# Kernel optimization log

Measured on AMD Instinct MI355X. Metric: run time of the kernel, lower is better.

Reference implementation:

```python
import jax, jax.numpy as jnp
import numpy as np

MOMENTUM = 0.5  # update_method='momentum'
EPS = 1e-12


def _l2norm(x):
    return x / jnp.sqrt(jnp.sum(x * x, axis=-1, keepdims=True) + EPS)


def setup_inputs() -> dict:
    key = jax.random.key(0)
    k1, k2, k3, k4, k5 = jax.random.split(key, 5)
    N, D, C, B = 200000, 256, 1000, 256
    inputs = _l2norm(jax.random.normal(k1, (B, D), dtype=jnp.float32))
    features = _l2norm(jax.random.normal(k2, (N, D), dtype=jnp.float32))
    cluster_mean = jax.random.normal(k3, (C, D), dtype=jnp.float32)
    labels = jax.random.randint(k4, (N,), 0, C)
    indexes = jax.random.randint(k5, (B,), 0, N)
    targets = labels[indexes]  # cluster id of each mini-batch sample
    return {
        "inputs": inputs,
        "features": features,
        "cluster_mean": cluster_mean,
        "indexes": indexes,
        "labels": labels,
        "targets": targets,
    }


def reference(inputs, features, cluster_mean, indexes, labels, targets):
    # HM.forward: logits against cluster centroids
    outputs = inputs @ cluster_mean.T  # [B, C]

    # HM.backward side effects (memory-bank maintenance), vectorized:
    # 1) momentum scatter update of the per-instance memory bank + L2 renorm
    new_rows = MOMENTUM * features[indexes] + (1.0 - MOMENTUM) * inputs
    new_rows = _l2norm(new_rows)
    feats = features.at[indexes].set(new_rows)

    # 2) naive cluster-mean recompute (get_mean_conv mean part) for touched clusters
    C = cluster_mean.shape[0]
    sums = jax.ops.segment_sum(feats, labels, num_segments=C)            # [C, D]
    cnts = jax.ops.segment_sum(jnp.ones((feats.shape[0],), feats.dtype), labels, num_segments=C)
    means = sums / jnp.maximum(cnts, 1.0)[:, None]
    touched = jnp.zeros((C,), dtype=bool).at[targets].set(True)
    new_cluster_mean = jnp.where(touched[:, None], means, cluster_mean)

    return outputs, feats, new_cluster_mean
```

## Files before the change

kernel.cpp:

```cpp
#include <hip/hip_runtime.h>

typedef float f32x4 __attribute__((ext_vector_type(4)));

#define B 256
#define D 256
#define N 200000
#define C 1000

#define K1_BLOCKS   2048
#define LOGITS_LO   0
#define NEWROWS_LO  256
#define TOUCH_BLK   512
#define HIST_LO     513
#define HIST_BLOCKS 64
#define COPY_LO     577
#define COPY_BLOCKS (K1_BLOCKS - COPY_LO)

#define WS_NEWROWS_OFF  0
#define WS_HIST_OFF     262144
#define WS_TOUCHED_OFF  266144
#define WS_OFFS_OFF     270144
#define WS_FILLPOS_OFF  274144
#define WS_ROWLIST_OFF  278144
#define ZERO_WORDS      (2 * C)

__global__ __launch_bounds__(256) void k0_zero(int* __restrict__ z) {
    int i = blockIdx.x * 256 + threadIdx.x;
    if (i < ZERO_WORDS) z[i] = 0;
}

__global__ __launch_bounds__(256) void k1_kernel(
    const float* __restrict__ inputs, const float* __restrict__ features,
    const float* __restrict__ cluster_mean, const int* __restrict__ indexes,
    const int* __restrict__ labels, const int* __restrict__ targets,
    float* __restrict__ out_logits, float* __restrict__ out_feats,
    float* __restrict__ new_rows, int* __restrict__ hist, int* __restrict__ touched)
{
    const int blk = blockIdx.x;
    const int t = threadIdx.x;

    if (blk >= COPY_LO) {
        const f32x4* src = (const f32x4*)features;
        f32x4*       dst = (f32x4*)out_feats;
        const int total4 = N * (D / 4);
        const int stride = COPY_BLOCKS * 256;
        int i = (blk - COPY_LO) * 256 + t;
        for (; i + 3 * stride < total4; i += 4 * stride) {
            f32x4 v0 = src[i];
            f32x4 v1 = src[i + stride];
            f32x4 v2 = src[i + 2 * stride];
            f32x4 v3 = src[i + 3 * stride];
            __builtin_nontemporal_store(v0, dst + i);
            __builtin_nontemporal_store(v1, dst + i + stride);
            __builtin_nontemporal_store(v2, dst + i + 2 * stride);
            __builtin_nontemporal_store(v3, dst + i + 3 * stride);
        }
        for (; i < total4; i += stride)
            __builtin_nontemporal_store(src[i], dst + i);
    } else if (blk < NEWROWS_LO) {
        __shared__ float sbuf[D];
        int b = blk - LOGITS_LO;
        sbuf[t] = inputs[b * D + t];
        __syncthreads();
        const f32x4* cmv = (const f32x4*)cluster_mean;
        for (int c = t; c < C; c += 256) {
            const f32x4* cm = cmv + (size_t)c * 64;
            float a0 = 0.f, a1 = 0.f, a2 = 0.f, a3 = 0.f;
            #pragma unroll 8
            for (int d4 = 0; d4 < 64; ++d4) {
                f32x4 v = cm[d4];
                const float* si = sbuf + d4 * 4;
                a0 += v.x * si[0];
                a1 += v.y * si[1];
                a2 += v.z * si[2];
                a3 += v.w * si[3];
            }
            out_logits[(size_t)b * C + c] = (a0 + a1) + (a2 + a3);
        }
    } else if (blk < TOUCH_BLK) {
        __shared__ float wpart[4];
        __shared__ float stot;
        int b = blk - NEWROWS_LO;
        int r = indexes[b];
        float x = 0.5f * features[(size_t)r * D + t] + 0.5f * inputs[b * D + t];
        float s = x * x;
        #pragma unroll
        for (int off = 32; off > 0; off >>= 1) s += __shfl_down(s, off);
        if ((t & 63) == 0) wpart[t >> 6] = s;
        __syncthreads();
        if (t == 0) stot = (wpart[0] + wpart[1]) + (wpart[2] + wpart[3]);
        __syncthreads();
        new_rows[b * D + t] = x / sqrtf(stot + 1e-12f);
    } else if (blk == TOUCH_BLK) {
        if (t < B) touched[targets[t]] = 1;
    } else {
        __shared__ int lh[C];
        for (int i = t; i < C; i += 256) lh[i] = 0;
        __syncthreads();
        const int stride = HIST_BLOCKS * 256;
        for (int i = (blk - HIST_LO) * 256 + t; i < N; i += stride)
            atomicAdd(&lh[labels[i]], 1);
        __syncthreads();
        for (int i = t; i < C; i += 256) {
            int v = lh[i];
            if (v) atomicAdd(&hist[i], v);
        }
    }
}

__global__ __launch_bounds__(256) void k2_kernel(
    const int* __restrict__ indexes, const float* __restrict__ new_rows,
    float* __restrict__ out_feats, const int* __restrict__ hist,
    int* __restrict__ offs, int* __restrict__ fillpos)
{
    const int blk = blockIdx.x;
    const int t = threadIdx.x;

    if (blk < 256) {
        __shared__ int sidx[B];
        __shared__ int lose;
        sidx[t] = indexes[t];
        if (t == 0) lose = 0;
        __syncthreads();
        int b = blk;
        int my = sidx[b];
        if (t > b && sidx[t] == my) lose = 1;
        __syncthreads();
        if (!lose) out_feats[(size_t)my * D + t] = new_rows[b * D + t];
    } else {
        __shared__ int swt[4];
        int base = t * 4;
        int h0 = (base + 0 < C) ? hist[base + 0] : 0;
        int h1 = (base + 1 < C) ? hist[base + 1] : 0;
        int h2 = (base + 2 < C) ? hist[base + 2] : 0;
        int h3 = (base + 3 < C) ? hist[base + 3] : 0;
        int tot = h0 + h1 + h2 + h3;
        int lane = t & 63;
        int scan = tot;
        #pragma unroll
        for (int off = 1; off < 64; off <<= 1) {
            int v = __shfl_up(scan, off);
            if (lane >= off) scan += v;
        }
        if (lane == 63) swt[t >> 6] = scan;
        __syncthreads();
        int wbase = 0;
        for (int i = 0; i < (t >> 6); ++i) wbase += swt[i];
        int excl = wbase + scan - tot;
        if (base + 0 < C) { offs[base + 0] = excl;                fillpos[base + 0] = excl; }
        if (base + 1 < C) { offs[base + 1] = excl + h0;           fillpos[base + 1] = excl + h0; }
        if (base + 2 < C) { offs[base + 2] = excl + h0 + h1;      fillpos[base + 2] = excl + h0 + h1; }
        if (base + 3 < C) { offs[base + 3] = excl + h0 + h1 + h2; fillpos[base + 3] = excl + h0 + h1 + h2; }
    }
}

__global__ __launch_bounds__(256) void fill_kernel(
    const int* __restrict__ labels, const int* __restrict__ touched,
    int* __restrict__ fillpos, int* __restrict__ rowlist)
{
    int i = blockIdx.x * 256 + threadIdx.x;
    if (i >= N) return;
    int lab = labels[i];
    if (touched[lab]) {
        int p = atomicAdd(&fillpos[lab], 1);
        rowlist[p] = i;
    }
}

__global__ __launch_bounds__(1024) void cm_kernel(
    const float* __restrict__ cluster_mean, const float* __restrict__ out_feats,
    const int* __restrict__ touched, const int* __restrict__ hist,
    const int* __restrict__ offs, const int* __restrict__ rowlist,
    float* __restrict__ out_cm)
{
    const int c = blockIdx.x;
    const int d = threadIdx.x & 255;
    const int k = threadIdx.x >> 8;
    if (!touched[c]) {
        if (k == 0) out_cm[(size_t)c * D + d] = cluster_mean[(size_t)c * D + d];
        return;
    }
    __shared__ float red[3][256];
    const int cnt = hist[c];
    const int off = offs[c];
    float acc = 0.0f;
    #pragma unroll 4
    for (int j = k; j < cnt; j += 4)
        acc += out_feats[(size_t)rowlist[off + j] * D + d];
    if (k > 0) red[k - 1][d] = acc;
    __syncthreads();
    if (k == 0) {
        float tot = acc + red[0][d] + red[1][d] + red[2][d];
        out_cm[(size_t)c * D + d] = tot / fmaxf((float)cnt, 1.0f);
    }
}

extern "C" void kernel_launch(void* const* d_in, const int* in_sizes, int n_in,
                              void* d_out, int out_size, void* d_ws, size_t ws_size,
                              hipStream_t stream) {
    const float* inputs       = (const float*)d_in[0];
    const float* features     = (const float*)d_in[1];
    const float* cluster_mean = (const float*)d_in[2];
    const int*   indexes      = (const int*)d_in[3];
    const int*   labels       = (const int*)d_in[4];
    const int*   targets      = (const int*)d_in[5];

    float* out_logits = (float*)d_out;
    float* out_feats  = out_logits + (size_t)B * C;
    float* out_cm     = out_feats + (size_t)N * D;

    char* ws = (char*)d_ws;
    float* new_rows = (float*)(ws + WS_NEWROWS_OFF);
    int*   hist     = (int*)(ws + WS_HIST_OFF);
    int*   touched  = (int*)(ws + WS_TOUCHED_OFF);
    int*   offs     = (int*)(ws + WS_OFFS_OFF);
    int*   fillpos  = (int*)(ws + WS_FILLPOS_OFF);
    int*   rowlist  = (int*)(ws + WS_ROWLIST_OFF);

    k0_zero<<<(ZERO_WORDS + 255) / 256, 256, 0, stream>>>((int*)(ws + WS_HIST_OFF));
    k1_kernel<<<K1_BLOCKS, 256, 0, stream>>>(inputs, features, cluster_mean,
                                             indexes, labels, targets,
                                             out_logits, out_feats, new_rows,
                                             hist, touched);
    k2_kernel<<<257, 256, 0, stream>>>(indexes, new_rows, out_feats,
                                       hist, offs, fillpos);
    fill_kernel<<<(N + 255) / 256, 256, 0, stream>>>(labels, touched, fillpos, rowlist);
    cm_kernel<<<C, 1024, 0, stream>>>(cluster_mean, out_feats, touched, hist,
                                      offs, rowlist, out_cm);
}
```

Baseline: 125.3 us.

## Compute cluster sums from original features plus delta correction for updated rows

The cluster-mean kernel now gathers rows from the input features buffer instead of the freshly written output bank. It then adds a correction term (new_row − old_row) for each scattered row whose label matches the cluster. k2 records each winning scattered row's index, label and batch slot into a compact list via an atomic counter, and its row scatter now uses nontemporal stores. The aim is to read from a buffer more likely to be cache-resident and not freshly overwritten. In exchange, every touched-cluster block scans the full write list and does extra loads, and floating-point summation order changes slightly.

```diff
diff --git a/kernel.cpp b/kernel.cpp
--- a/kernel.cpp
+++ b/kernel.cpp
@@ -19,10 +19,14 @@
 #define WS_NEWROWS_OFF  0
 #define WS_HIST_OFF     262144
 #define WS_TOUCHED_OFF  266144
-#define WS_OFFS_OFF     270144
-#define WS_FILLPOS_OFF  274144
-#define WS_ROWLIST_OFF  278144
-#define ZERO_WORDS      (2 * C)
+#define WS_NW_OFF       270144
+#define WS_OFFS_OFF     270148
+#define WS_FILLPOS_OFF  274148
+#define WS_WROW_OFF     278148
+#define WS_WLAB_OFF     279172
+#define WS_WB_OFF       280196
+#define WS_ROWLIST_OFF  281220
+#define ZERO_WORDS      (2 * C + 1)
 
 __global__ __launch_bounds__(256) void k0_zero(int* __restrict__ z) {
     int i = blockIdx.x * 256 + threadIdx.x;
@@ -109,9 +113,11 @@
 }
 
 __global__ __launch_bounds__(256) void k2_kernel(
-    const int* __restrict__ indexes, const float* __restrict__ new_rows,
-    float* __restrict__ out_feats, const int* __restrict__ hist,
-    int* __restrict__ offs, int* __restrict__ fillpos)
+    const int* __restrict__ indexes, const int* __restrict__ labels,
+    const float* __restrict__ new_rows, float* __restrict__ out_feats,
+    const int* __restrict__ hist, int* __restrict__ offs, int* __restrict__ fillpos,
+    int* __restrict__ nw, int* __restrict__ w_row, int* __restrict__ w_lab,
+    int* __restrict__ w_b)
 {
     const int blk = blockIdx.x;
     const int t = threadIdx.x;
@@ -126,7 +132,15 @@
         int my = sidx[b];
         if (t > b && sidx[t] == my) lose = 1;
         __syncthreads();
-        if (!lose) out_feats[(size_t)my * D + t] = new_rows[b * D + t];
+        if (!lose) {
+            __builtin_nontemporal_store(new_rows[b * D + t], &out_feats[(size_t)my * D + t]);
+            if (t == 0) {
+                int p = atomicAdd(nw, 1);
+                w_row[p] = my;
+                w_lab[p] = labels[my];
+                w_b[p] = b;
+            }
+        }
     } else {
         __shared__ int swt[4];
         int base = t * 4;
@@ -168,10 +182,12 @@
 }
 
 __global__ __launch_bounds__(1024) void cm_kernel(
-    const float* __restrict__ cluster_mean, const float* __restrict__ out_feats,
-    const int* __restrict__ touched, const int* __restrict__ hist,
-    const int* __restrict__ offs, const int* __restrict__ rowlist,
-    float* __restrict__ out_cm)
+    const float* __restrict__ cluster_mean, const float* __restrict__ features,
+    const float* __restrict__ new_rows, const int* __restrict__ touched,
+    const int* __restrict__ hist, const int* __restrict__ offs,
+    const int* __restrict__ rowlist, const int* __restrict__ nw,
+    const int* __restrict__ w_row, const int* __restrict__ w_lab,
+    const int* __restrict__ w_b, float* __restrict__ out_cm)
 {
     const int c = blockIdx.x;
     const int d = threadIdx.x & 255;
@@ -186,7 +202,12 @@
     float acc = 0.0f;
     #pragma unroll 4
     for (int j = k; j < cnt; j += 4)
-        acc += out_feats[(size_t)rowlist[off + j] * D + d];
+        acc += features[(size_t)rowlist[off + j] * D + d];
+    const int nwv = *nw;
+    for (int j = k; j < nwv; j += 4) {
+        if (w_lab[j] == c)
+            acc += new_rows[w_b[j] * D + d] - features[(size_t)w_row[j] * D + d];
+    }
     if (k > 0) red[k - 1][d] = acc;
     __syncthreads();
     if (k == 0) {
@@ -213,8 +234,12 @@
     float* new_rows = (float*)(ws + WS_NEWROWS_OFF);
     int*   hist     = (int*)(ws + WS_HIST_OFF);
     int*   touched  = (int*)(ws + WS_TOUCHED_OFF);
+    int*   nw       = (int*)(ws + WS_NW_OFF);
     int*   offs     = (int*)(ws + WS_OFFS_OFF);
     int*   fillpos  = (int*)(ws + WS_FILLPOS_OFF);
+    int*   w_row    = (int*)(ws + WS_WROW_OFF);
+    int*   w_lab    = (int*)(ws + WS_WLAB_OFF);
+    int*   w_b      = (int*)(ws + WS_WB_OFF);
     int*   rowlist  = (int*)(ws + WS_ROWLIST_OFF);
 
     k0_zero<<<(ZERO_WORDS + 255) / 256, 256, 0, stream>>>((int*)(ws + WS_HIST_OFF));
@@ -222,9 +247,10 @@
                                              indexes, labels, targets,
                                              out_logits, out_feats, new_rows,
                                              hist, touched);
-    k2_kernel<<<257, 256, 0, stream>>>(indexes, new_rows, out_feats,
-                                       hist, offs, fillpos);
+    k2_kernel<<<257, 256, 0, stream>>>(indexes, labels, new_rows, out_feats,
+                                       hist, offs, fillpos, nw, w_row, w_lab, w_b);
     fill_kernel<<<(N + 255) / 256, 256, 0, stream>>>(labels, touched, fillpos, rowlist);
-    cm_kernel<<<C, 1024, 0, stream>>>(cluster_mean, out_feats, touched, hist,
-                                      offs, rowlist, out_cm);
-}
+    cm_kernel<<<C, 1024, 0, stream>>>(cluster_mean, features, new_rows, touched,
+                                      hist, offs, rowlist, nw, w_row, w_lab, w_b,
+                                      out_cm);
+}
```

Result: no change. 124.7 us (-0.5%).

## Merge post-copy stages into one kernel with in-kernel flag synchronization

Applied to the files above, without the earlier changes.

Collapses the zero, patch, scan, fill and cluster-mean kernels into one launch. Blocks wait on global flags (scan done, fill done) using spin loops, which removes several launch gaps. Histogram partials are written per block instead of atomically, so the zeroing kernel is no longer needed. The cluster-mean stage now reads the original features and adds a correction for rows that were overwritten, so it no longer depends on the patched out_feats. The spin-waits assume all producer blocks get scheduled before consumers and would deadlock if residency does not allow that. The mean blocks also now use 256 threads instead of 1024.

```diff
diff --git a/kernel.cpp b/kernel.cpp
--- a/kernel.cpp
+++ b/kernel.cpp
@@ -8,43 +8,51 @@
 #define C 1000
 
 #define K1_BLOCKS   2048
-#define LOGITS_LO   0
-#define NEWROWS_LO  256
-#define TOUCH_BLK   512
-#define HIST_LO     513
+#define COPY_BLOCKS 1471
+#define LOGITS_LO   1471
+#define NEWROWS_LO  1727
+#define WIN_BLK     1983
+#define HIST_LO     1984
 #define HIST_BLOCKS 64
-#define COPY_LO     577
-#define COPY_BLOCKS (K1_BLOCKS - COPY_LO)
+
+#define PATCH_LO    1
+#define FILL_LO     257
+#define FILL_BLOCKS 782
+#define CM_LO       (FILL_LO + FILL_BLOCKS)
+#define K2_BLOCKS   (CM_LO + C)
 
 #define WS_NEWROWS_OFF  0
-#define WS_HIST_OFF     262144
-#define WS_TOUCHED_OFF  266144
-#define WS_OFFS_OFF     270144
-#define WS_FILLPOS_OFF  274144
-#define WS_ROWLIST_OFF  278144
-#define ZERO_WORDS      (2 * C)
-
-__global__ __launch_bounds__(256) void k0_zero(int* __restrict__ z) {
-    int i = blockIdx.x * 256 + threadIdx.x;
-    if (i < ZERO_WORDS) z[i] = 0;
-}
+#define WS_NW_OFF       262144
+#define WS_FLAG_OFF     262148
+#define WS_DONE_OFF     262152
+#define WS_OFFS_OFF     262156
+#define WS_FILLPOS_OFF  266156
+#define WS_CNTS_OFF     270156
+#define WS_TOUCHED_OFF  274156
+#define WS_WROW_OFF     278156
+#define WS_WLAB_OFF     279180
+#define WS_WB_OFF       280204
+#define WS_HB_OFF       281228
+#define WS_ROWLIST_OFF  537228
 
 __global__ __launch_bounds__(256) void k1_kernel(
     const float* __restrict__ inputs, const float* __restrict__ features,
     const float* __restrict__ cluster_mean, const int* __restrict__ indexes,
     const int* __restrict__ labels, const int* __restrict__ targets,
     float* __restrict__ out_logits, float* __restrict__ out_feats,
-    float* __restrict__ new_rows, int* __restrict__ hist, int* __restrict__ touched)
+    float* __restrict__ new_rows, int* __restrict__ hb, int* __restrict__ touched,
+    int* __restrict__ nw, int* __restrict__ w_row, int* __restrict__ w_lab,
+    int* __restrict__ w_b, int* __restrict__ flag, int* __restrict__ done)
 {
     const int blk = blockIdx.x;
     const int t = threadIdx.x;
 
-    if (blk >= COPY_LO) {
+    if (blk < COPY_BLOCKS) {
         const f32x4* src = (const f32x4*)features;
         f32x4*       dst = (f32x4*)out_feats;
         const int total4 = N * (D / 4);
         const int stride = COPY_BLOCKS * 256;
-        int i = (blk - COPY_LO) * 256 + t;
+        int i = blk * 256 + t;
         for (; i + 3 * stride < total4; i += 4 * stride) {
             f32x4 v0 = src[i];
             f32x4 v1 = src[i + stride];
@@ -77,7 +85,7 @@
             }
             out_logits[(size_t)b * C + c] = (a0 + a1) + (a2 + a3);
         }
-    } else if (blk < TOUCH_BLK) {
+    } else if (blk < WIN_BLK) {
         __shared__ float wpart[4];
         __shared__ float stot;
         int b = blk - NEWROWS_LO;
@@ -91,49 +99,63 @@
         if (t == 0) stot = (wpart[0] + wpart[1]) + (wpart[2] + wpart[3]);
         __syncthreads();
         new_rows[b * D + t] = x / sqrtf(stot + 1e-12f);
-    } else if (blk == TOUCH_BLK) {
-        if (t < B) touched[targets[t]] = 1;
+    } else if (blk == WIN_BLK) {
+        __shared__ int sidx[B];
+        __shared__ int cnt;
+        for (int i = t; i < C; i += 256) touched[i] = 0;
+        sidx[t] = indexes[t];
+        if (t == 0) { cnt = 0; *flag = 0; *done = 0; }
+        __syncthreads();
+        touched[targets[t]] = 1;
+        bool win = true;
+        for (int j = t + 1; j < B; ++j)
+            if (sidx[j] == sidx[t]) { win = false; break; }
+        if (win) {
+            int p = atomicAdd(&cnt, 1);
+            int r = sidx[t];
+            w_row[p] = r;
+            w_lab[p] = labels[r];
+            w_b[p] = t;
+        }
+        __syncthreads();
+        if (t == 0) *nw = cnt;
     } else {
         __shared__ int lh[C];
         for (int i = t; i < C; i += 256) lh[i] = 0;
         __syncthreads();
+        const int hb_i = blk - HIST_LO;
         const int stride = HIST_BLOCKS * 256;
-        for (int i = (blk - HIST_LO) * 256 + t; i < N; i += stride)
+        for (int i = hb_i * 256 + t; i < N; i += stride)
             atomicAdd(&lh[labels[i]], 1);
         __syncthreads();
-        for (int i = t; i < C; i += 256) {
-            int v = lh[i];
-            if (v) atomicAdd(&hist[i], v);
-        }
+        for (int i = t; i < C; i += 256) hb[hb_i * C + i] = lh[i];
     }
 }
 
-__global__ __launch_bounds__(256) void k2_kernel(
-    const int* __restrict__ indexes, const float* __restrict__ new_rows,
-    float* __restrict__ out_feats, const int* __restrict__ hist,
-    int* __restrict__ offs, int* __restrict__ fillpos)
+__global__ __launch_bounds__(256, 8) void k2_kernel(
+    const float* __restrict__ cluster_mean, const float* __restrict__ features,
+    const float* __restrict__ new_rows, const int* __restrict__ labels,
+    float* __restrict__ out_feats, float* __restrict__ out_cm,
+    const int* __restrict__ hb, int* __restrict__ offs, int* __restrict__ fillpos,
+    int* __restrict__ cnts, const int* __restrict__ touched,
+    const int* __restrict__ nw, const int* __restrict__ w_row,
+    const int* __restrict__ w_lab, const int* __restrict__ w_b,
+    int* __restrict__ rowlist, int* __restrict__ flag, int* __restrict__ done)
 {
     const int blk = blockIdx.x;
     const int t = threadIdx.x;
 
-    if (blk < 256) {
-        __shared__ int sidx[B];
-        __shared__ int lose;
-        sidx[t] = indexes[t];
-        if (t == 0) lose = 0;
-        __syncthreads();
-        int b = blk;
-        int my = sidx[b];
-        if (t > b && sidx[t] == my) lose = 1;
-        __syncthreads();
-        if (!lose) out_feats[(size_t)my * D + t] = new_rows[b * D + t];
-    } else {
+    if (blk == 0) {
         __shared__ int swt[4];
         int base = t * 4;
-        int h0 = (base + 0 < C) ? hist[base + 0] : 0;
-        int h1 = (base + 1 < C) ? hist[base + 1] : 0;
-        int h2 = (base + 2 < C) ? hist[base + 2] : 0;
-        int h3 = (base + 3 < C) ? hist[base + 3] : 0;
+        int h0 = 0, h1 = 0, h2 = 0, h3 = 0;
+        for (int i = 0; i < HIST_BLOCKS; ++i) {
+            const int* row = hb + i * C;
+            if (base + 0 < C) h0 += row[base + 0];
+            if (base + 1 < C) h1 += row[base + 1];
+            if (base + 2 < C) h2 += row[base + 2];
+            if (base + 3 < C) h3 += row[base + 3];
+        }
         int tot = h0 + h1 + h2 + h3;
         int lane = t & 63;
         int scan = tot;
@@ -147,51 +169,68 @@
         int wbase = 0;
         for (int i = 0; i < (t >> 6); ++i) wbase += swt[i];
         int excl = wbase + scan - tot;
-        if (base + 0 < C) { offs[base + 0] = excl;                fillpos[base + 0] = excl; }
-        if (base + 1 < C) { offs[base + 1] = excl + h0;           fillpos[base + 1] = excl + h0; }
-        if (base + 2 < C) { offs[base + 2] = excl + h0 + h1;      fillpos[base + 2] = excl + h0 + h1; }
-        if (base + 3 < C) { offs[base + 3] = excl + h0 + h1 + h2; fillpos[base + 3] = excl + h0 + h1 + h2; }
-    }
-}
-
-__global__ __launch_bounds__(256) void fill_kernel(
-    const int* __restrict__ labels, const int* __restrict__ touched,
-    int* __restrict__ fillpos, int* __restrict__ rowlist)
-{
-    int i = blockIdx.x * 256 + threadIdx.x;
-    if (i >= N) return;
-    int lab = labels[i];
-    if (touched[lab]) {
-        int p = atomicAdd(&fillpos[lab], 1);
-        rowlist[p] = i;
-    }
-}
-
-__global__ __launch_bounds__(1024) void cm_kernel(
-    const float* __restrict__ cluster_mean, const float* __restrict__ out_feats,
-    const int* __restrict__ touched, const int* __restrict__ hist,
-    const int* __restrict__ offs, const int* __restrict__ rowlist,
-    float* __restrict__ out_cm)
-{
-    const int c = blockIdx.x;
-    const int d = threadIdx.x & 255;
-    const int k = threadIdx.x >> 8;
-    if (!touched[c]) {
-        if (k == 0) out_cm[(size_t)c * D + d] = cluster_mean[(size_t)c * D + d];
-        return;
-    }
-    __shared__ float red[3][256];
-    const int cnt = hist[c];
-    const int off = offs[c];
-    float acc = 0.0f;
-    #pragma unroll 4
-    for (int j = k; j < cnt; j += 4)
-        acc += out_feats[(size_t)rowlist[off + j] * D + d];
-    if (k > 0) red[k - 1][d] = acc;
-    __syncthreads();
-    if (k == 0) {
-        float tot = acc + red[0][d] + red[1][d] + red[2][d];
-        out_cm[(size_t)c * D + d] = tot / fmaxf((float)cnt, 1.0f);
+        if (base + 0 < C) { offs[base + 0] = excl;                fillpos[base + 0] = excl;                cnts[base + 0] = h0; }
+        if (base + 1 < C) { offs[base + 1] = excl + h0;           fillpos[base + 1] = excl + h0;           cnts[base + 1] = h1; }
+        if (base + 2 < C) { offs[base + 2] = excl + h0 + h1;      fillpos[base + 2] = excl + h0 + h1;      cnts[base + 2] = h2; }
+        if (base + 3 < C) { offs[base + 3] = excl + h0 + h1 + h2; fillpos[base + 3] = excl + h0 + h1 + h2; cnts[base + 3] = h3; }
+        __threadfence();
+        __syncthreads();
+        if (t == 0) atomicExch(flag, 1);
+    } else if (blk < FILL_LO) {
+        int q = blk - PATCH_LO;
+        if (q < *nw)
+            out_feats[(size_t)w_row[q] * D + t] = new_rows[w_b[q] * D + t];
+    } else if (blk < CM_LO) {
+        if (t == 0) {
+            while (atomicAdd(flag, 0) == 0) __builtin_amdgcn_s_sleep(8);
+        }
+        __syncthreads();
+        __threadfence();
+        int i = (blk - FILL_LO) * 256 + t;
+        if (i < N) {
+            int lab = labels[i];
+            if (touched[lab]) {
+                int p = atomicAdd(&fillpos[lab], 1);
+                rowlist[p] = i;
+            }
+        }
+        __threadfence();
+        __syncthreads();
+        if (t == 0) atomicAdd(done, 1);
+    } else {
+        int c = blk - CM_LO;
+        if (!touched[c]) {
+            out_cm[(size_t)c * D + t] = cluster_mean[(size_t)c * D + t];
+            return;
+        }
+        if (t == 0) {
+            while (atomicAdd(done, 0) < FILL_BLOCKS) __builtin_amdgcn_s_sleep(8);
+        }
+        __syncthreads();
+        __threadfence();
+        const int cnt = cnts[c];
+        const int off = offs[c];
+        float a0 = 0.f, a1 = 0.f, a2 = 0.f, a3 = 0.f;
+        int j = 0;
+        for (; j + 3 < cnt; j += 4) {
+            int r0 = rowlist[off + j + 0];
+            int r1 = rowlist[off + j + 1];
+            int r2 = rowlist[off + j + 2];
+            int r3 = rowlist[off + j + 3];
+            a0 += features[(size_t)r0 * D + t];
+            a1 += features[(size_t)r1 * D + t];
+            a2 += features[(size_t)r2 * D + t];
+            a3 += features[(size_t)r3 * D + t];
+        }
+        for (; j < cnt; ++j)
+            a0 += features[(size_t)rowlist[off + j] * D + t];
+        float acc = (a0 + a1) + (a2 + a3);
+        const int nwv = *nw;
+        for (int q = 0; q < nwv; ++q) {
+            if (w_lab[q] == c)
+                acc += new_rows[w_b[q] * D + t] - features[(size_t)w_row[q] * D + t];
+        }
+        out_cm[(size_t)c * D + t] = acc / fmaxf((float)cnt, 1.0f);
     }
 }
 
@@ -211,20 +250,27 @@
 
     char* ws = (char*)d_ws;
     float* new_rows = (float*)(ws + WS_NEWROWS_OFF);
-    int*   hist     = (int*)(ws + WS_HIST_OFF);
-    int*   touched  = (int*)(ws + WS_TOUCHED_OFF);
+    int*   nw       = (int*)(ws + WS_NW_OFF);
+    int*   flag     = (int*)(ws + WS_FLAG_OFF);
+    int*   done     = (int*)(ws + WS_DONE_OFF);
     int*   offs     = (int*)(ws + WS_OFFS_OFF);
     int*   fillpos  = (int*)(ws + WS_FILLPOS_OFF);
+    int*   cnts     = (int*)(ws + WS_CNTS_OFF);
+    int*   touched  = (int*)(ws + WS_TOUCHED_OFF);
+    int*   w_row    = (int*)(ws + WS_WROW_OFF);
+    int*   w_lab    = (int*)(ws + WS_WLAB_OFF);
+    int*   w_b      = (int*)(ws + WS_WB_OFF);
+    int*   hb       = (int*)(ws + WS_HB_OFF);
     int*   rowlist  = (int*)(ws + WS_ROWLIST_OFF);
 
-    k0_zero<<<(ZERO_WORDS + 255) / 256, 256, 0, stream>>>((int*)(ws + WS_HIST_OFF));
     k1_kernel<<<K1_BLOCKS, 256, 0, stream>>>(inputs, features, cluster_mean,
                                              indexes, labels, targets,
                                              out_logits, out_feats, new_rows,
-                                             hist, touched);
-    k2_kernel<<<257, 256, 0, stream>>>(indexes, new_rows, out_feats,
-                                       hist, offs, fillpos);
-    fill_kernel<<<(N + 255) / 256, 256, 0, stream>>>(labels, touched, fillpos, rowlist);
-    cm_kernel<<<C, 1024, 0, stream>>>(cluster_mean, out_feats, touched, hist,
-                                      offs, rowlist, out_cm);
+                                             hb, touched, nw, w_row, w_lab, w_b,
+                                             flag, done);
+    k2_kernel<<<K2_BLOCKS, 256, 0, stream>>>(cluster_mean, features, new_rows,
+                                             labels, out_feats, out_cm,
+                                             hb, offs, fillpos, cnts, touched,
+                                             nw, w_row, w_lab, w_b, rowlist,
+                                             flag, done);
 }
```

New measurement: 335.7 us. 2.68x slower.
